# Performance work log

Hardware: AMD Instinct MI355X
Metric: run time of the kernel (lower is better)

Reference implementation:

```python
import jax, jax.numpy as jnp
import numpy as np

# Hyperparameters matching init_kwargs
NOISE_POWER = 1.0
DT = 0.01
T_MAX = 10.0
LAM = 1.0
RHO = 1.0
N_BLOCKS = 64
N_LINKS = 1024


def setup_inputs() -> dict:
    key = jax.random.key(0)
    k1, k2 = jax.random.split(key)
    # Transmit powers per block / link, strictly positive
    powers = jax.random.uniform(k1, (N_BLOCKS, N_LINKS), dtype=jnp.float32) + 0.1
    # Link gain matrix: strong diagonal (direct link), weak off-diagonal interference
    pathloss = jax.random.uniform(k2, (N_LINKS, N_LINKS), dtype=jnp.float32) * 0.01 \
               + jnp.eye(N_LINKS, dtype=jnp.float32)
    return {"powers": powers, "pathloss": pathloss}


def _depthwise_corr(Q, q):
    """torch F.conv1d(Q, q[:,None,:], padding=T-1, groups=L)[:, :T].
    Q, q: [L, T] -> [L, T]. Cross-correlation semantics (same as torch conv1d)."""
    L, T = Q.shape
    out = jax.lax.conv_general_dilated(
        Q[None],                 # [1, L, T]
        q[:, None, :],           # [L, 1, T] depthwise kernels
        window_strides=(1,),
        padding=[(T - 1, T - 1)],
        feature_group_count=L,
        dimension_numbers=("NCH", "OIH", "NCH"),
    )
    return out[0, :, :T]


def reference(powers, pathloss):
    N, L = powers.shape
    t_array = jnp.arange(0.0, T_MAX, DT, dtype=jnp.float32)      # [T]
    pow2t = jnp.exp2(t_array)                                    # 2^t
    pow2t_1 = pow2t - 1.0                                        # 2^t - 1

    # signal[n, i, j] = pathloss[i, j] * powers[n, j]
    signal = pathloss[None, :, :] * powers[:, None, :]           # [N, L, L]
    y_ii = jnp.diagonal(signal, axis1=1, axis2=2)                # [N, L]
    y_ij = jnp.sum(signal, axis=2) - y_ii                        # interference
    sinr = y_ii / (y_ij + NOISE_POWER)                           # [N, L]

    ln2 = jnp.log(jnp.float32(2.0))

    # First-block outage CDF over t
    Q1 = 1.0 - jnp.exp(-pow2t_1[None, :] * sinr[0][:, None])     # [L, T]

    def step(Q_prev, sinr_n):
        # per-link kernel q_ii(t) = exp(-(2^t-1) s) * 2^t * s * ln2
        q = jnp.exp(-pow2t_1[None, :] * sinr_n[:, None]) \
            * pow2t[None, :] * sinr_n[:, None] * ln2             # [L, T]
        Qn = _depthwise_corr(Q_prev, q) * DT                     # [L, T]
        return Qn, Qn[:, -1]

    _, tail = jax.lax.scan(step, Q1, sinr[1:])                   # tail: [N-1, L]
    outa = jnp.concatenate([Q1[:, -1][None, :], tail], axis=0)   # [N, L]

    E = powers[0] + jnp.sum(powers[1:] * outa[: N - 1], axis=0)  # [L]
    D = 1.0 + jnp.sum(outa[: N - 1], axis=0)                     # [L]
    loss = jnp.sum(E) + LAM * jnp.sum(outa[N - 1]) + RHO * jnp.sum(D)
    return loss
```

## Files before the change

### kernel.cpp

```cpp
#include <hip/hip_runtime.h>
#include <math.h>

#define T_N   1000
#define L_N   1024
#define N_B   64
#define PADU  288
#define LOG2E 1.4426950408889634f
#define LN2   0.6931471805599453f
#define DT_F  0.01f
#define KCUT  5.0f

typedef unsigned int u32;
typedef _Float16 h2_t __attribute__((ext_vector_type(2)));

__device__ __forceinline__ float dot2f(u32 t, u32 w, float c) {
#if __has_builtin(__builtin_amdgcn_fdot2)
    return __builtin_amdgcn_fdot2(__builtin_bit_cast(h2_t, t),
                                  __builtin_bit_cast(h2_t, w), c, false);
#else
    h2_t a = __builtin_bit_cast(h2_t, t), b = __builtin_bit_cast(h2_t, w);
    return fmaf((float)a.x, (float)b.x, fmaf((float)a.y, (float)b.y, c));
#endif
}

__device__ __forceinline__ u32 pk(float lo, float hi) {
    h2_t v; v.x = (_Float16)lo; v.y = (_Float16)hi;
    return __builtin_bit_cast(u32, v);
}

__global__ __launch_bounds__(256) void sinr_kernel(const float* __restrict__ powers,
                                                   const float* __restrict__ pathloss,
                                                   float* __restrict__ sinr,
                                                   float* __restrict__ out) {
    const int tid  = threadIdx.x;
    const int wv   = tid >> 6;
    const int lane = tid & 63;
    const int i    = 2 * blockIdx.x + (wv & 1);
    const int n0   = 32 * (wv >> 1);

    if (blockIdx.x == 0 && tid == 0) out[0] = 0.f;

    const float4* row4g = (const float4*)(pathloss + i * L_N);
    float4 row[4];
    #pragma unroll
    for (int k = 0; k < 4; ++k) row[k] = row4g[lane + 64 * k];
    const float pii = pathloss[i * L_N + i];

    for (int nn = 0; nn < 32; nn += 4) {
        float part[4];
        #pragma unroll
        for (int u = 0; u < 4; ++u) {
            const float4* pr4 = (const float4*)(powers + (n0 + nn + u) * L_N);
            float s = 0.f;
            #pragma unroll
            for (int k = 0; k < 4; ++k) {
                float4 p = pr4[lane + 64 * k];
                s = fmaf(row[k].x, p.x, s);
                s = fmaf(row[k].y, p.y, s);
                s = fmaf(row[k].z, p.z, s);
                s = fmaf(row[k].w, p.w, s);
            }
            part[u] = s;
        }
        #pragma unroll
        for (int off = 32; off > 0; off >>= 1) {
            part[0] += __shfl_down(part[0], off, 64);
            part[1] += __shfl_down(part[1], off, 64);
            part[2] += __shfl_down(part[2], off, 64);
            part[3] += __shfl_down(part[3], off, 64);
        }
        if (lane == 0) {
            #pragma unroll
            for (int u = 0; u < 4; ++u) {
                const int n = n0 + nn + u;
                float yii = pii * powers[n * L_N + i];
                sinr[n * L_N + i] = yii / (part[u] - yii + 1.0f);
            }
        }
    }
}

#define D8(W0, W1, W2, W3, TE, TO) do {                                      \
    a0 = dot2f(TE, W0, a0); a1 = dot2f(TO, W0, a1);                          \
    a2 = dot2f(TE, W1, a2); a3 = dot2f(TO, W1, a3);                          \
    a4 = dot2f(TE, W2, a4); a5 = dot2f(TO, W2, a5);                          \
    a6 = dot2f(TE, W3, a6); a7 = dot2f(TO, W3, a7);                          \
} while (0)

__global__ __launch_bounds__(128) void scan_kernel(const float* __restrict__ powers,
                                                   const float* __restrict__ sinr,
                                                   float* __restrict__ out) {
    __shared__ __align__(16) float p2t[1024];
    __shared__ __align__(16) u32 P[2][PADU + 512];
    __shared__ __align__(16) u32 T[512];
    __shared__ float sv[N_B];
    __shared__ float tails[N_B];
    __shared__ u32 bridge;

    const int l    = blockIdx.x;
    const int tid  = threadIdx.x;
    const int lane = tid & 63;
    const int wr   = ((tid >> 6) ^ (blockIdx.x & 1) ^ ((blockIdx.x >> 3) & 1)) & 1;

    #pragma unroll
    for (int m = 0; m < 2; ++m) {
        const int jq = tid + 128 * m;
        float4 v;
        v.x = exp2f(0.01f * (float)(4 * jq + 0));
        v.y = exp2f(0.01f * (float)(4 * jq + 1));
        v.z = exp2f(0.01f * (float)(4 * jq + 2));
        v.w = exp2f(0.01f * (float)(4 * jq + 3));
        *(float4*)&p2t[4 * jq] = v;
    }
    if (tid < N_B) { sv[tid] = sinr[tid * L_N + l]; tails[tid] = 0.f; }
    for (int i = tid; i < PADU; i += 128) { P[0][i] = 0; P[1][i] = 0; }
    if (tid >= 125) *(uint4*)&T[4 * tid] = make_uint4(0u, 0u, 0u, 0u);
    __syncthreads();

    {
        const float s0l = sv[0] * LOG2E;
        const int jb = 8 * tid;
        float q[9];
        #pragma unroll
        for (int ii = 0; ii < 9; ++ii) {
            const int j = jb - 1 + ii;
            float v = 0.f;
            if (j >= 0 && j < T_N) v = 1.f - exp2f((1.f - p2t[j]) * s0l);
            q[ii] = v;
        }
        uint4 w;
        w.x = pk(q[1], q[0]); w.y = pk(q[3], q[2]);
        w.z = pk(q[5], q[4]); w.w = pk(q[7], q[6]);
        *(uint4*)&P[0][PADU + 4 * tid] = w;
        if (tid == 124) tails[0] = q[8];
    }
    __syncthreads();

    const int NB   = wr ? 126 : 64;
    const int j0   = 512 * wr + 8 * lane;
    const int s4   = j0 >> 3;
    const int jmxW = 512 * wr + 511;

    int A  = 0;
    int cb = 0;
    for (int n = 1; n < N_B; ++n) {
        const float s = sv[n];
        const int kstar = (int)(100.f * log2f(KCUT / s)) + 1;
        int dmin = 999 - kstar; if (dmin < 0) dmin = 0;
        const int Aprev = A;
        A += dmin;
        if (A > 999) break;
        const int k0 = dmin >> 3;
        int kend = ((jmxW - Aprev) >> 3) + 1;
        if (kend > NB) kend = NB;
        int kcap = ((1023 - Aprev) >> 3) + 2;
        if (kcap > 124) kcap = 124;

        if (n >= 2 && wr == 1 && lane == 0)
            ((unsigned short*)&P[cb][PADU + 256])[1] = (unsigned short)bridge;
        if (tid >= k0 && tid <= kcap) {
            const float sl   = s * LOG2E;
            const float smul = s * LN2 * DT_F;
            const int t8 = 8 * tid;
            float4 pa = *(const float4*)&p2t[996 - t8];
            float4 pb = *(const float4*)&p2t[992 - t8];
            float r0 = smul * pa.w * exp2f((1.f - pa.w) * sl);
            float r1 = smul * pa.z * exp2f((1.f - pa.z) * sl);
            float r2 = smul * pa.y * exp2f((1.f - pa.y) * sl);
            float r3 = smul * pa.x * exp2f((1.f - pa.x) * sl);
            float r4 = smul * pb.w * exp2f((1.f - pb.w) * sl);
            float r5 = smul * pb.z * exp2f((1.f - pb.z) * sl);
            float r6 = smul * pb.y * exp2f((1.f - pb.y) * sl);
            float r7 = smul * pb.x * exp2f((1.f - pb.x) * sl);
            uint4 tw;
            tw.x = pk(r0, r1); tw.y = pk(r2, r3);
            tw.z = pk(r4, r5); tw.w = pk(r6, r7);
            *(uint4*)&T[4 * tid] = tw;
        }
        __syncthreads();

        const u32*   Pc = &P[cb][PADU];
        const uint4* P4 = (const uint4*)Pc;
        const uint4* T4 = (const uint4*)T;

        float a0 = 0.f, a1 = 0.f, a2 = 0.f, a3 = 0.f;
        float a4 = 0.f, a5 = 0.f, a6 = 0.f, a7 = 0.f;

        if (k0 < kend) {
            uint4 wc = P4[s4 - k0], wn = P4[s4 - k0 - 1];
            uint4 tc = T4[k0],      tn = T4[k0 + 1];

            #pragma unroll 2
            for (int k = k0; k < kend; ++k) {
                uint4 wnn = P4[s4 - k - 2];
                uint4 tnn = T4[k + 2];
                u32 al;
                al = (tc.x >> 16) | (tc.y << 16);
                D8(wc.x, wc.y, wc.z, wc.w, tc.x, al);
                al = (tc.y >> 16) | (tc.z << 16);
                D8(wn.w, wc.x, wc.y, wc.z, tc.y, al);
                al = (tc.z >> 16) | (tc.w << 16);
                D8(wn.z, wn.w, wc.x, wc.y, tc.z, al);
                al = (tc.w >> 16) | (tn.x << 16);
                D8(wn.y, wn.z, wn.w, wc.x, tc.w, al);
                wc = wn; wn = wnn; tc = tn; tn = tnn;
            }
        }

        {
            float qm1 = __shfl_up(a7, 1, 64);
            if (lane == 0) qm1 = 0.f;
            float b0 = (j0 + 0 < T_N) ? a0 : 0.f;
            float b1 = (j0 + 1 < T_N) ? a1 : 0.f;
            float b2 = (j0 + 2 < T_N) ? a2 : 0.f;
            float b3 = (j0 + 3 < T_N) ? a3 : 0.f;
            float b4 = (j0 + 4 < T_N) ? a4 : 0.f;
            float b5 = (j0 + 5 < T_N) ? a5 : 0.f;
            float b6 = (j0 + 6 < T_N) ? a6 : 0.f;
            float bm = (j0     <= T_N) ? qm1 : 0.f;
            uint4 w;
            w.x = pk(b0, bm); w.y = pk(b2, b1);
            w.z = pk(b4, b3); w.w = pk(b6, b5);
            *(uint4*)&P[cb ^ 1][PADU + 4 * s4] = w;
            if (wr == 1 && lane == 60) tails[n] = a7;
            if (wr == 0 && lane == 63)
                bridge = (u32)__builtin_bit_cast(unsigned short, (_Float16)a7);
        }
        __syncthreads();
        cb ^= 1;
    }
    __syncthreads();

    if (tid < N_B) {
        float tl   = tails[tid];
        float term = (tid < N_B - 1) ? tl * (powers[(tid + 1) * L_N + l] + 1.0f) : tl;
        if (tid == 0) term += powers[l] + 1.0f;
        #pragma unroll
        for (int off = 32; off > 0; off >>= 1) term += __shfl_down(term, off, 64);
        if (tid == 0) atomicAdd(out, term);
    }
}

extern "C" void kernel_launch(void* const* d_in, const int* in_sizes, int n_in,
                              void* d_out, int out_size, void* d_ws, size_t ws_size,
                              hipStream_t stream) {
    const float* powers   = (const float*)d_in[0];
    const float* pathloss = (const float*)d_in[1];
    float* sinr = (float*)d_ws;
    float* out  = (float*)d_out;

    sinr_kernel<<<dim3(L_N / 2), dim3(256), 0, stream>>>(powers, pathloss, sinr, out);
    scan_kernel<<<dim3(L_N), dim3(128), 0, stream>>>(powers, sinr, out);
}
```

Measured before the change: 38.64 us.

## Schedule scan blocks by estimated per-link cost to balance load across CUs

```diff
diff --git a/kernel.cpp b/kernel.cpp
--- a/kernel.cpp
+++ b/kernel.cpp
@@ -9,6 +9,7 @@
 #define LN2   0.6931471805599453f
 #define DT_F  0.01f
 #define KCUT  5.0f
+#define STEP_OVH 24
 
 typedef unsigned int u32;
 typedef _Float16 h2_t __attribute__((ext_vector_type(2)));
@@ -31,7 +32,9 @@
 __global__ __launch_bounds__(256) void sinr_kernel(const float* __restrict__ powers,
                                                    const float* __restrict__ pathloss,
                                                    float* __restrict__ sinr,
-                                                   float* __restrict__ out) {
+                                                   float* __restrict__ out,
+                                                   int* __restrict__ cost) {
+    __shared__ float svb[2][N_B];
     const int tid  = threadIdx.x;
     const int wv   = tid >> 6;
     const int lane = tid & 63;
@@ -74,10 +77,47 @@
             for (int u = 0; u < 4; ++u) {
                 const int n = n0 + nn + u;
                 float yii = pii * powers[n * L_N + i];
-                sinr[n * L_N + i] = yii / (part[u] - yii + 1.0f);
+                float v   = yii / (part[u] - yii + 1.0f);
+                sinr[n * L_N + i] = v;
+                svb[wv & 1][n] = v;
             }
         }
     }
+    __syncthreads();
+
+    if (tid < 2) {
+        const float* svp = svb[tid];
+        int A = 0, cv = 0;
+        for (int n = 1; n < N_B; ++n) {
+            const float s = svp[n];
+            const int kstar = (int)(100.f * log2f(KCUT / s)) + 1;
+            int dmin = 999 - kstar; if (dmin < 0) dmin = 0;
+            const int Aprev = A;
+            A += dmin;
+            if (A > 999) break;
+            const int k0 = dmin >> 3;
+            int kend = ((1023 - Aprev) >> 3) + 1; if (kend > 126) kend = 126;
+            int trip = kend - k0; if (trip < 0) trip = 0;
+            cv += trip + STEP_OVH;
+        }
+        cost[2 * blockIdx.x + tid] = cv;
+    }
+}
+
+__global__ __launch_bounds__(64) void rank_kernel(const int* __restrict__ cost,
+                                                  int* __restrict__ linkOfRank) {
+    __shared__ int cl[L_N];
+    const int l = 64 * blockIdx.x + threadIdx.x;
+    for (int j = threadIdx.x; j < L_N; j += 64) cl[j] = cost[j];
+    __syncthreads();
+    const int c = cl[l];
+    int cnt = 0;
+    #pragma unroll 8
+    for (int j = 0; j < L_N; ++j) {
+        const int cj = cl[j];
+        cnt += (cj > c) || (cj == c && j < l);
+    }
+    linkOfRank[cnt] = l;
 }
 
 #define D8(W0, W1, W2, W3, TE, TO) do {                                      \
@@ -89,7 +129,8 @@
 
 __global__ __launch_bounds__(128) void scan_kernel(const float* __restrict__ powers,
                                                    const float* __restrict__ sinr,
-                                                   float* __restrict__ out) {
+                                                   float* __restrict__ out,
+                                                   const int* __restrict__ linkOfRank) {
     __shared__ __align__(16) float p2t[1024];
     __shared__ __align__(16) u32 P[2][PADU + 512];
     __shared__ __align__(16) u32 T[512];
@@ -97,10 +138,15 @@
     __shared__ float tails[N_B];
     __shared__ u32 bridge;
 
-    const int l    = blockIdx.x;
+    const int b    = blockIdx.x;
+    const int cu   = b & 255;
+    const int slot = b >> 8;
+    const int rank = slot * 256 + ((slot & 1) ? (255 - cu) : cu);
+    const int l    = linkOfRank[rank];
+
     const int tid  = threadIdx.x;
     const int lane = tid & 63;
-    const int wr   = ((tid >> 6) ^ (blockIdx.x & 1) ^ ((blockIdx.x >> 3) & 1)) & 1;
+    const int wr   = ((tid >> 6) ^ (b & 1)) & 1;
 
     #pragma unroll
     for (int m = 0; m < 2; ++m) {
@@ -246,9 +292,12 @@
                               hipStream_t stream) {
     const float* powers   = (const float*)d_in[0];
     const float* pathloss = (const float*)d_in[1];
-    float* sinr = (float*)d_ws;
-    float* out  = (float*)d_out;
-
-    sinr_kernel<<<dim3(L_N / 2), dim3(256), 0, stream>>>(powers, pathloss, sinr, out);
-    scan_kernel<<<dim3(L_N), dim3(128), 0, stream>>>(powers, sinr, out);
-}
+    float* sinr       = (float*)d_ws;
+    int*   cost       = (int*)(sinr + N_B * L_N);
+    int*   linkOfRank = cost + L_N;
+    float* out        = (float*)d_out;
+
+    sinr_kernel<<<dim3(L_N / 2), dim3(256), 0, stream>>>(powers, pathloss, sinr, out, cost);
+    rank_kernel<<<dim3(16), dim3(64), 0, stream>>>(cost, linkOfRank);
+    scan_kernel<<<dim3(L_N), dim3(128), 0, stream>>>(powers, sinr, out, linkOfRank);
+}
```

New measurement: 66.15 us. +71.2%, slower.

## Fuse SINR computation into scan kernel and drop separate launch

Applied to the files above, without the earlier changes.

```diff
diff --git a/kernel.cpp b/kernel.cpp
--- a/kernel.cpp
+++ b/kernel.cpp
@@ -28,58 +28,6 @@
     return __builtin_bit_cast(u32, v);
 }
 
-__global__ __launch_bounds__(256) void sinr_kernel(const float* __restrict__ powers,
-                                                   const float* __restrict__ pathloss,
-                                                   float* __restrict__ sinr,
-                                                   float* __restrict__ out) {
-    const int tid  = threadIdx.x;
-    const int wv   = tid >> 6;
-    const int lane = tid & 63;
-    const int i    = 2 * blockIdx.x + (wv & 1);
-    const int n0   = 32 * (wv >> 1);
-
-    if (blockIdx.x == 0 && tid == 0) out[0] = 0.f;
-
-    const float4* row4g = (const float4*)(pathloss + i * L_N);
-    float4 row[4];
-    #pragma unroll
-    for (int k = 0; k < 4; ++k) row[k] = row4g[lane + 64 * k];
-    const float pii = pathloss[i * L_N + i];
-
-    for (int nn = 0; nn < 32; nn += 4) {
-        float part[4];
-        #pragma unroll
-        for (int u = 0; u < 4; ++u) {
-            const float4* pr4 = (const float4*)(powers + (n0 + nn + u) * L_N);
-            float s = 0.f;
-            #pragma unroll
-            for (int k = 0; k < 4; ++k) {
-                float4 p = pr4[lane + 64 * k];
-                s = fmaf(row[k].x, p.x, s);
-                s = fmaf(row[k].y, p.y, s);
-                s = fmaf(row[k].z, p.z, s);
-                s = fmaf(row[k].w, p.w, s);
-            }
-            part[u] = s;
-        }
-        #pragma unroll
-        for (int off = 32; off > 0; off >>= 1) {
-            part[0] += __shfl_down(part[0], off, 64);
-            part[1] += __shfl_down(part[1], off, 64);
-            part[2] += __shfl_down(part[2], off, 64);
-            part[3] += __shfl_down(part[3], off, 64);
-        }
-        if (lane == 0) {
-            #pragma unroll
-            for (int u = 0; u < 4; ++u) {
-                const int n = n0 + nn + u;
-                float yii = pii * powers[n * L_N + i];
-                sinr[n * L_N + i] = yii / (part[u] - yii + 1.0f);
-            }
-        }
-    }
-}
-
 #define D8(W0, W1, W2, W3, TE, TO) do {                                      \
     a0 = dot2f(TE, W0, a0); a1 = dot2f(TO, W0, a1);                          \
     a2 = dot2f(TE, W1, a2); a3 = dot2f(TO, W1, a3);                          \
@@ -88,9 +36,10 @@
 } while (0)
 
 __global__ __launch_bounds__(128) void scan_kernel(const float* __restrict__ powers,
-                                                   const float* __restrict__ sinr,
+                                                   const float* __restrict__ pathloss,
                                                    float* __restrict__ out) {
     __shared__ __align__(16) float p2t[1024];
+    __shared__ __align__(16) float rowL[1024];
     __shared__ __align__(16) u32 P[2][PADU + 512];
     __shared__ __align__(16) u32 T[512];
     __shared__ float sv[N_B];
@@ -100,21 +49,66 @@
     const int l    = blockIdx.x;
     const int tid  = threadIdx.x;
     const int lane = tid & 63;
-    const int wr   = ((tid >> 6) ^ (blockIdx.x & 1) ^ ((blockIdx.x >> 3) & 1)) & 1;
-
-    #pragma unroll
-    for (int m = 0; m < 2; ++m) {
-        const int jq = tid + 128 * m;
-        float4 v;
-        v.x = exp2f(0.01f * (float)(4 * jq + 0));
-        v.y = exp2f(0.01f * (float)(4 * jq + 1));
-        v.z = exp2f(0.01f * (float)(4 * jq + 2));
-        v.w = exp2f(0.01f * (float)(4 * jq + 3));
-        *(float4*)&p2t[4 * jq] = v;
-    }
-    if (tid < N_B) { sv[tid] = sinr[tid * L_N + l]; tails[tid] = 0.f; }
+    const int wv   = tid >> 6;
+    const int wr   = (wv ^ (blockIdx.x & 1) ^ ((blockIdx.x >> 3) & 1)) & 1;
+
+    {
+        const float4* rg = (const float4*)(pathloss + l * L_N);
+        *(float4*)&rowL[4 * tid]       = rg[tid];
+        *(float4*)&rowL[4 * (tid+128)] = rg[tid + 128];
+        #pragma unroll
+        for (int m = 0; m < 2; ++m) {
+            const int jq = tid + 128 * m;
+            float4 v;
+            v.x = exp2f(0.01f * (float)(4 * jq + 0));
+            v.y = exp2f(0.01f * (float)(4 * jq + 1));
+            v.z = exp2f(0.01f * (float)(4 * jq + 2));
+            v.w = exp2f(0.01f * (float)(4 * jq + 3));
+            *(float4*)&p2t[4 * jq] = v;
+        }
+    }
     for (int i = tid; i < PADU; i += 128) { P[0][i] = 0; P[1][i] = 0; }
     if (tid >= 125) *(uint4*)&T[4 * tid] = make_uint4(0u, 0u, 0u, 0u);
+    __syncthreads();
+
+    {
+        float4 row[4];
+        #pragma unroll
+        for (int k = 0; k < 4; ++k) row[k] = *(const float4*)&rowL[4 * (lane + 64 * k)];
+        const float pii = rowL[l];
+        const int n0 = 32 * wv;
+        for (int nn = 0; nn < 32; nn += 2) {
+            float part[2];
+            #pragma unroll
+            for (int u = 0; u < 2; ++u) {
+                const float4* pr4 = (const float4*)(powers + (n0 + nn + u) * L_N);
+                float s = 0.f;
+                #pragma unroll
+                for (int k = 0; k < 4; ++k) {
+                    float4 p = pr4[lane + 64 * k];
+                    s = fmaf(row[k].x, p.x, s);
+                    s = fmaf(row[k].y, p.y, s);
+                    s = fmaf(row[k].z, p.z, s);
+                    s = fmaf(row[k].w, p.w, s);
+                }
+                part[u] = s;
+            }
+            #pragma unroll
+            for (int off = 32; off > 0; off >>= 1) {
+                part[0] += __shfl_down(part[0], off, 64);
+                part[1] += __shfl_down(part[1], off, 64);
+            }
+            if (lane == 0) {
+                #pragma unroll
+                for (int u = 0; u < 2; ++u) {
+                    const int n = n0 + nn + u;
+                    float yii = pii * powers[n * L_N + l];
+                    sv[n] = yii / (part[u] - yii + 1.0f);
+                }
+            }
+        }
+        if (tid < N_B) tails[tid] = 0.f;
+    }
     __syncthreads();
 
     {
@@ -246,9 +240,8 @@
                               hipStream_t stream) {
     const float* powers   = (const float*)d_in[0];
     const float* pathloss = (const float*)d_in[1];
-    float* sinr = (float*)d_ws;
-    float* out  = (float*)d_out;
-
-    sinr_kernel<<<dim3(L_N / 2), dim3(256), 0, stream>>>(powers, pathloss, sinr, out);
-    scan_kernel<<<dim3(L_N), dim3(128), 0, stream>>>(powers, sinr, out);
-}
+    float* out = (float*)d_out;
+
+    hipMemsetAsync(out, 0, sizeof(float), stream);
+    scan_kernel<<<dim3(L_N), dim3(128), 0, stream>>>(powers, pathloss, out);
+}
```

Result: slower. 40.96 us (+6.0%).
